# Kernel optimization log

Measured on AMD Instinct MI355X. Metric: run time of the kernel, lower is better.

The kernel has to match this reference:

```python
import jax, jax.numpy as jnp
import numpy as np

B, S, D, H, E = 4, 2048, 1024, 4096, 8


def setup_inputs() -> dict:
    key = jax.random.key(0)
    ks = jax.random.split(key, 8)
    w = lambda k, shape: (jax.random.normal(k, shape, jnp.float32) * 0.02)
    return {
        "x": jax.random.normal(ks[0], (B, S, D), jnp.float32),
        "noise_eps": jax.random.normal(ks[1], (B, S, E), jnp.float32),
        "Wg": w(ks[2], (D, E)), "bg": jnp.zeros((E,), jnp.float32),
        "Wn": w(ks[3], (D, E)), "bn": jnp.zeros((E,), jnp.float32),
        "W1": w(ks[4], (E, D, H)), "b1": jnp.zeros((E, H), jnp.float32),
        "W2": w(ks[5], (E, H, D)), "b2": jnp.zeros((E, D), jnp.float32),
        "top_k": 2,
    }


def reference(x, noise_eps, Wg, bg, Wn, bn, W1, b1, W2, b2, top_k):
    b, s, d = x.shape
    e = Wg.shape[1]
    xt = x.reshape(-1, d)            # [T, D] flattened tokens
    eps = noise_eps.reshape(-1, e)   # [T, E]

    # Noisy top-k router
    logits = xt @ Wg + bg                                   # [T, E]
    noisy = logits + eps * jax.nn.softplus(xt @ Wn + bn)    # [T, E]
    top_vals, top_idx = jax.lax.top_k(noisy, top_k)         # [T, k]

    # sparse logits: -inf everywhere except top-k, then softmax -> 0 gate off-topk
    rows = jnp.arange(xt.shape[0])[:, None]
    sparse = jnp.full_like(noisy, -jnp.inf).at[rows, top_idx].set(top_vals)
    gate = jax.nn.softmax(sparse, axis=-1)                  # [T, E], zeros off-topk

    # Expert MLPs (exact GELU, as nn.GELU default); gate==0 off-topk reproduces
    # the masked gather/scatter combine of the original exactly.
    out = jnp.zeros_like(xt)
    for i in range(e):  # small fixed expert count
        h = jax.nn.gelu(xt @ W1[i] + b1[i], approximate=False)  # [T, H]
        o = h @ W2[i] + b2[i]                                   # [T, D]
        out = out + o * gate[:, i:i + 1]
    return out.reshape(b, s, d)
```

## Files before the change

kernel.cpp:

```cpp
#include <hip/hip_runtime.h>
#include <hip/hip_bf16.h>
#include <cmath>

#define T_TOK 8192
#define E_NUM 8
#define D_DIM 1024
#define H_DIM 4096

typedef __attribute__((ext_vector_type(4))) short bf16x4;
typedef __attribute__((ext_vector_type(8))) short bf16x8;
typedef __attribute__((ext_vector_type(4))) float f32x4;

__device__ __forceinline__ unsigned short f2bf(float f) {
  union { float f; unsigned u; } v; v.f = f;
  unsigned r = v.u + 0x7fffu + ((v.u >> 16) & 1u);
  return (unsigned short)(r >> 16);
}

__device__ __forceinline__ void gload_lds16(const void* g, void* l) {
  __builtin_amdgcn_global_load_lds(
      (const __attribute__((address_space(1))) unsigned int*)g,
      (__attribute__((address_space(3))) unsigned int*)l, 16, 0, 0);
}


__global__ void __launch_bounds__(256) cvt_x_kernel(const float* __restrict__ x,
                                                    ushort* __restrict__ xb) {
  int i = blockIdx.x * 256 + threadIdx.x;
  float4 v = ((const float4*)x)[i];
  ushort4 o;
  o.x = f2bf(v.x); o.y = f2bf(v.y); o.z = f2bf(v.z); o.w = f2bf(v.w);
  int u = i & 7;
  int oi = (i & ~7) | (((u & 3) << 1) | (u >> 2));
  ((ushort4*)xb)[oi] = o;
}

__global__ void __launch_bounds__(256) transpose_cvt_kernel(
    const float* __restrict__ src, ushort* __restrict__ dst, int K, int N) {
  __shared__ __align__(16) float tile[64][68];
  size_t eoff = (size_t)blockIdx.z * K * N;
  int n0 = blockIdx.x * 64, k0 = blockIdx.y * 64;
  int t = threadIdx.x;
  int kr = t >> 4, nc = (t & 15) * 4;
#pragma unroll
  for (int i = 0; i < 4; ++i) {
    float4 v = *(const float4*)(src + eoff + (size_t)(k0 + kr + i * 16) * N + n0 + nc);
    *(float4*)&tile[kr + i * 16][nc] = v;
  }
  __syncthreads();
  int n = t >> 3, s = t & 7, g = s >> 2, p = s & 3;
#pragma unroll
  for (int j = 0; j < 2; ++j) {
    int nn = n + j * 32;
    union { bf16x8 v8; ushort e[8]; } o;
#pragma unroll
    for (int h = 0; h < 2; ++h)
#pragma unroll
      for (int r = 0; r < 4; ++r) {
        int k = g * 32 + h * 16 + p * 4 + r;
        o.e[h * 4 + r] = f2bf(tile[k][nn]);
      }
    *(bf16x8*)(dst + eoff + (size_t)(n0 + nn) * K + k0 + g * 32 + p * 8) = o.v8;
  }
}

__global__ void __launch_bounds__(256) router_kernel(
    const float* __restrict__ x, const float* __restrict__ eps,
    const float* __restrict__ Wg, const float* __restrict__ bg,
    const float* __restrict__ Wn, const float* __restrict__ bn,
    int* __restrict__ tok, float* __restrict__ gateL, int* __restrict__ cnt) {
  int lane = threadIdx.x & 63;
  int t = blockIdx.x * 4 + (threadIdx.x >> 6);
  float ag[8], an[8];
#pragma unroll
  for (int e = 0; e < 8; ++e) { ag[e] = 0.f; an[e] = 0.f; }
  const float* xr = x + (size_t)t * D_DIM;
#pragma unroll 4
  for (int i = 0; i < 16; ++i) {
    int d = lane + i * 64;
    float xv = xr[d];
    const float4* g4 = (const float4*)(Wg + d * 8);
    const float4* n4 = (const float4*)(Wn + d * 8);
    float4 ga = g4[0], gb = g4[1], na = n4[0], nb = n4[1];
    ag[0] += xv * ga.x; ag[1] += xv * ga.y; ag[2] += xv * ga.z; ag[3] += xv * ga.w;
    ag[4] += xv * gb.x; ag[5] += xv * gb.y; ag[6] += xv * gb.z; ag[7] += xv * gb.w;
    an[0] += xv * na.x; an[1] += xv * na.y; an[2] += xv * na.z; an[3] += xv * na.w;
    an[4] += xv * nb.x; an[5] += xv * nb.y; an[6] += xv * nb.z; an[7] += xv * nb.w;
  }
#pragma unroll
  for (int off = 32; off > 0; off >>= 1) {
#pragma unroll
    for (int e = 0; e < 8; ++e) {
      ag[e] += __shfl_xor(ag[e], off);
      an[e] += __shfl_xor(an[e], off);
    }
  }
  if (lane == 0) {
    float noisy[8];
#pragma unroll
    for (int e = 0; e < 8; ++e) {
      float lg = ag[e] + bg[e];
      float ln = an[e] + bn[e];
      float sp = (ln > 20.f) ? ln : log1pf(expf(ln));
      noisy[e] = lg + eps[(size_t)t * 8 + e] * sp;
    }
    int i0 = 0; float v0 = noisy[0];
#pragma unroll
    for (int e = 1; e < 8; ++e) if (noisy[e] > v0) { v0 = noisy[e]; i0 = e; }
    int i1 = -1; float v1 = -1e30f;
#pragma unroll
    for (int e = 0; e < 8; ++e) if (e != i0 && noisy[e] > v1) { v1 = noisy[e]; i1 = e; }
    float ee = expf(v1 - v0);
    float g0 = 1.f / (1.f + ee);
    float g1 = ee / (1.f + ee);
    int p0 = atomicAdd(cnt + i0, 1);
    int p1 = atomicAdd(cnt + i1, 1);
    tok[i0 * T_TOK + p0] = t * 2;     gateL[i0 * T_TOK + p0] = g0;
    tok[i1 * T_TOK + p1] = t * 2 + 1; gateL[i1 * T_TOK + p1] = g1;
  }
}

template <int KD, int NC, bool FIRST>
__global__ void __launch_bounds__(256) moe_gemm_kernel(
    const ushort* __restrict__ Abase, const ushort* __restrict__ Bt,
    const float* __restrict__ bias, const int* __restrict__ tok,
    const float* __restrict__ gateL, const int* __restrict__ cnt,
    ushort* __restrict__ hbuf, float* __restrict__ out) {
  constexpr int MT = T_TOK / 128;
  constexpr int NT = NC / 128;
  int nwg = MT * NT * E_NUM;
  int q8 = nwg >> 3;
  int bid = blockIdx.x;
  int wg = (bid & 7) * q8 + (bid >> 3);
  int m_t = wg % MT;
  int n_t = (wg / MT) % NT;
  int e = wg / (MT * NT);

  int c = cnt[e];
  int m0 = m_t * 128;
  if (m0 >= c) return;
  int n0 = n_t * 128;

  __shared__ __align__(16) ushort As[128 * 64];
  __shared__ __align__(16) ushort Bs[128 * 64];
  int tid = threadIdx.x;
  int lane = tid & 63, wave = tid >> 6;
  int wr = (wave >> 1) * 64, wc = (wave & 1) * 64;
  const int* tokE = tok + e * T_TOK;
  const ushort* Be = Bt + (size_t)e * NC * KD;

  int srow = tid >> 3, scol = tid & 7;
  const ushort* asrc[4]; const ushort* bsrc[4];
#pragma unroll
  for (int p = 0; p < 4; ++p) {
    int r = p * 32 + srow;
    int pi = m0 + r;
    int ar = 0;
    if (pi < c) { int tsv = tokE[pi]; ar = FIRST ? (tsv >> 1) : tsv; }
    int sl = (scol ^ (r & 7)) * 8;
    asrc[p] = Abase + (size_t)ar * KD + sl;
    bsrc[p] = Be + (size_t)(n0 + r) * KD + sl;
  }

  f32x4 acc[4][4];
#pragma unroll
  for (int i = 0; i < 4; ++i)
#pragma unroll
    for (int j = 0; j < 4; ++j) {
      f32x4 z = {0.f, 0.f, 0.f, 0.f};
      acc[i][j] = z;
    }

  int r16 = lane & 15;
  int q = lane >> 4;
  int rr = lane & 7;
  int s0 = (q ^ rr) << 4;

  for (int kt = 0; kt < KD / 64; ++kt) {
    __syncthreads();
#pragma unroll
    for (int p = 0; p < 4; ++p)
      gload_lds16(asrc[p] + kt * 64, (char*)As + p * 4096 + tid * 16);
#pragma unroll
    for (int p = 0; p < 4; ++p)
      gload_lds16(bsrc[p] + kt * 64, (char*)Bs + p * 4096 + tid * 16);
    __syncthreads();

#pragma unroll
    for (int ks = 0; ks < 2; ++ks) {
      const int so = s0 ^ (ks << 6);
      bf16x8 af[4], bfr[4];
#pragma unroll
      for (int i = 0; i < 4; ++i) {
        af[i]  = *(const bf16x8*)((const char*)As + (wr + i * 16 + r16) * 128 + so);
        bfr[i] = *(const bf16x8*)((const char*)Bs + (wc + i * 16 + r16) * 128 + so);
      }
#pragma unroll
      for (int mi = 0; mi < 4; ++mi)
#pragma unroll
        for (int ni = 0; ni < 4; ++ni)
          acc[mi][ni] = __builtin_amdgcn_mfma_f32_16x16x32_bf16(
              af[mi], bfr[ni], acc[mi][ni], 0, 0, 0);
    }
  }

  const float* be = bias + (size_t)e * NC;
#pragma unroll
  for (int mi = 0; mi < 4; ++mi) {
#pragma unroll
    for (int r = 0; r < 4; ++r) {
      int rowl = wr + mi * 16 + q * 4 + r;
      int p = m0 + rowl;
      if (p < c) {
        int tsv = tokE[p];
        if (FIRST) {
          ushort* hrow = hbuf + (size_t)tsv * H_DIM;
#pragma unroll
          for (int ni = 0; ni < 4; ++ni) {
            int col = n0 + wc + ni * 16 + r16;
            float v = acc[mi][ni][r] + be[col];
            v = 0.5f * v * (1.f + erff(v * 0.70710678118654752f));
            int pos = ((r16 >> 2) & 3) * 8 + (ni & 1) * 4 + (r16 & 3);
            hrow[(col & ~31) + pos] = f2bf(v);
          }
        } else {
          float g = gateL[e * T_TOK + p];
          float* orow = out + (size_t)(tsv >> 1) * D_DIM;
#pragma unroll
          for (int ni = 0; ni < 4; ++ni) {
            int col = n0 + wc + ni * 16 + r16;
            float v = acc[mi][ni][r] + be[col];
            atomicAdd(&orow[col], g * v);
          }
        }
      }
    }
  }
}

extern "C" void kernel_launch(void* const* d_in, const int* in_sizes, int n_in,
                              void* d_out, int out_size, void* d_ws, size_t ws_size,
                              hipStream_t stream) {
  const float* x   = (const float*)d_in[0];
  const float* eps = (const float*)d_in[1];
  const float* Wg  = (const float*)d_in[2];
  const float* bg  = (const float*)d_in[3];
  const float* Wn  = (const float*)d_in[4];
  const float* bn  = (const float*)d_in[5];
  const float* W1  = (const float*)d_in[6];
  const float* b1  = (const float*)d_in[7];
  const float* W2  = (const float*)d_in[8];
  const float* b2  = (const float*)d_in[9];
  float* out = (float*)d_out;

  const size_t nXB = (size_t)T_TOK * D_DIM;
  const size_t nW1 = (size_t)E_NUM * D_DIM * H_DIM;
  const size_t nHB = (size_t)T_TOK * 2 * H_DIM;
  ushort* xb   = (ushort*)d_ws;
  ushort* W1T  = xb + nXB;
  ushort* W2T  = W1T + nW1;
  ushort* hbuf = W2T + nW1;
  int*   tok   = (int*)(hbuf + nHB);
  float* gateL = (float*)(tok + E_NUM * T_TOK);
  int*   cnt   = (int*)(gateL + E_NUM * T_TOK);
  size_t need = (size_t)((char*)(cnt + 8) - (char*)d_ws);
  if (ws_size < need) return;

  hipMemsetAsync(cnt, 0, 8 * sizeof(int), stream);
  hipMemsetAsync(out, 0, (size_t)out_size * sizeof(float), stream);

  cvt_x_kernel<<<(int)(nXB / 4 / 256), 256, 0, stream>>>(x, xb);
  transpose_cvt_kernel<<<dim3(H_DIM / 64, D_DIM / 64, E_NUM), 256, 0, stream>>>(
      W1, W1T, D_DIM, H_DIM);
  transpose_cvt_kernel<<<dim3(D_DIM / 64, H_DIM / 64, E_NUM), 256, 0, stream>>>(
      W2, W2T, H_DIM, D_DIM);
  router_kernel<<<T_TOK / 4, 256, 0, stream>>>(x, eps, Wg, bg, Wn, bn, tok, gateL, cnt);
  moe_gemm_kernel<D_DIM, H_DIM, true>
      <<<(T_TOK / 128) * (H_DIM / 128) * E_NUM, 256, 0, stream>>>(
          xb, W1T, b1, tok, gateL, cnt, hbuf, out);
  moe_gemm_kernel<H_DIM, D_DIM, false>
      <<<(T_TOK / 128) * (D_DIM / 128) * E_NUM, 256, 0, stream>>>(
          hbuf, W2T, b2, tok, gateL, cnt, hbuf, out);
}
```

Measured before the change: 1.294 ms.

## Double-buffer LDS tiles to overlap global loads with MFMA compute

Adds a second LDS buffer for the A and B tiles. The next k-tile is prefetched with global_load_lds while the MFMAs run on the current one, and the loop now needs one barrier per iteration instead of two. Launch bounds now request two blocks per CU. LDS use doubles to 64KB per block, which may limit occupancy. Correctness depends on the barrier draining the async LDS loads before the buffer is read.

Result: slower. 1.395 ms (+7.8%).

```diff
diff --git a/kernel.cpp b/kernel.cpp
--- a/kernel.cpp
+++ b/kernel.cpp
@@ -121,13 +121,14 @@
 }
 
 template <int KD, int NC, bool FIRST>
-__global__ void __launch_bounds__(256) moe_gemm_kernel(
+__global__ void __launch_bounds__(256, 2) moe_gemm_kernel(
     const ushort* __restrict__ Abase, const ushort* __restrict__ Bt,
     const float* __restrict__ bias, const int* __restrict__ tok,
     const float* __restrict__ gateL, const int* __restrict__ cnt,
     ushort* __restrict__ hbuf, float* __restrict__ out) {
   constexpr int MT = T_TOK / 128;
   constexpr int NT = NC / 128;
+  constexpr int NKT = KD / 64;
   int nwg = MT * NT * E_NUM;
   int q8 = nwg >> 3;
   int bid = blockIdx.x;
@@ -141,8 +142,8 @@
   if (m0 >= c) return;
   int n0 = n_t * 128;
 
-  __shared__ __align__(16) ushort As[128 * 64];
-  __shared__ __align__(16) ushort Bs[128 * 64];
+  __shared__ __align__(16) ushort As[2][128 * 64];
+  __shared__ __align__(16) ushort Bs[2][128 * 64];
   int tid = threadIdx.x;
   int lane = tid & 63, wave = tid >> 6;
   int wr = (wave >> 1) * 64, wc = (wave & 1) * 64;
@@ -176,24 +177,32 @@
   int rr = lane & 7;
   int s0 = (q ^ rr) << 4;
 
-  for (int kt = 0; kt < KD / 64; ++kt) {
-    __syncthreads();
-#pragma unroll
-    for (int p = 0; p < 4; ++p)
-      gload_lds16(asrc[p] + kt * 64, (char*)As + p * 4096 + tid * 16);
-#pragma unroll
-    for (int p = 0; p < 4; ++p)
-      gload_lds16(bsrc[p] + kt * 64, (char*)Bs + p * 4096 + tid * 16);
-    __syncthreads();
-
+#pragma unroll
+  for (int p = 0; p < 4; ++p) {
+    gload_lds16(asrc[p], (char*)As[0] + p * 4096 + tid * 16);
+    gload_lds16(bsrc[p], (char*)Bs[0] + p * 4096 + tid * 16);
+  }
+  __syncthreads();
+
+  int cur = 0;
+  for (int kt = 0; kt < NKT; ++kt) {
+    if (kt + 1 < NKT) {
+#pragma unroll
+      for (int p = 0; p < 4; ++p) {
+        gload_lds16(asrc[p] + (kt + 1) * 64, (char*)As[cur ^ 1] + p * 4096 + tid * 16);
+        gload_lds16(bsrc[p] + (kt + 1) * 64, (char*)Bs[cur ^ 1] + p * 4096 + tid * 16);
+      }
+    }
+    const char* Ab = (const char*)As[cur];
+    const char* Bb = (const char*)Bs[cur];
 #pragma unroll
     for (int ks = 0; ks < 2; ++ks) {
       const int so = s0 ^ (ks << 6);
       bf16x8 af[4], bfr[4];
 #pragma unroll
       for (int i = 0; i < 4; ++i) {
-        af[i]  = *(const bf16x8*)((const char*)As + (wr + i * 16 + r16) * 128 + so);
-        bfr[i] = *(const bf16x8*)((const char*)Bs + (wc + i * 16 + r16) * 128 + so);
+        af[i]  = *(const bf16x8*)(Ab + (wr + i * 16 + r16) * 128 + so);
+        bfr[i] = *(const bf16x8*)(Bb + (wc + i * 16 + r16) * 128 + so);
       }
 #pragma unroll
       for (int mi = 0; mi < 4; ++mi)
@@ -202,6 +211,8 @@
           acc[mi][ni] = __builtin_amdgcn_mfma_f32_16x16x32_bf16(
               af[mi], bfr[ni], acc[mi][ni], 0, 0, 0);
     }
+    __syncthreads();
+    cur ^= 1;
   }
 
   const float* be = bias + (size_t)e * NC;
```
